# Optimization experiments

Measured on AMD Instinct MI355X. Metric: run time of the kernel, lower is better.

The kernel has to match this reference:

```python
import jax, jax.numpy as jnp
import numpy as np

EMBED_DIM = 512
NUM_HEADS = 8
HEAD_DIM = EMBED_DIM // NUM_HEADS
EDGE_HIDDEN = 512
B, L = 2, 512


def setup_inputs() -> dict:
    key = jax.random.key(0)
    ks = jax.random.split(key, 16)
    s = 0.02
    inp = {
        "query": jax.random.normal(ks[0], (B, L, EMBED_DIM), jnp.float32),
        "key_in": jax.random.normal(ks[1], (B, L, EMBED_DIM), jnp.float32),
        "value": jax.random.normal(ks[2], (B, L, EMBED_DIM), jnp.float32),
        "edge_representation": jax.random.normal(ks[3], (B, L, L), jnp.float32),
        # projection weights stored as [in, out]: y = x @ W + b
        "Wq": jax.random.normal(ks[4], (EMBED_DIM, EMBED_DIM), jnp.float32) * s,
        "bq": jnp.zeros((EMBED_DIM,), jnp.float32),
        "Wk": jax.random.normal(ks[5], (EMBED_DIM, EMBED_DIM), jnp.float32) * s,
        "bk": jnp.zeros((EMBED_DIM,), jnp.float32),
        "Wv": jax.random.normal(ks[6], (EMBED_DIM, EMBED_DIM), jnp.float32) * s,
        "bv": jnp.zeros((EMBED_DIM,), jnp.float32),
        "Wo": jax.random.normal(ks[7], (EMBED_DIM, EMBED_DIM), jnp.float32) * s,
        "bo": jnp.zeros((EMBED_DIM,), jnp.float32),
        # edge MLP: Linear(1 -> 512) -> ReLU -> Linear(512 -> num_heads)
        "We1": jax.random.normal(ks[8], (1, EDGE_HIDDEN), jnp.float32) * s,
        "be1": jnp.zeros((EDGE_HIDDEN,), jnp.float32),
        "We2": jax.random.normal(ks[9], (EDGE_HIDDEN, NUM_HEADS), jnp.float32) * s,
        "be2": jnp.zeros((NUM_HEADS,), jnp.float32),
    }
    return inp


def reference(query, key_in, value, edge_representation,
              Wq, bq, Wk, bk, Wv, bv, Wo, bo, We1, be1, We2, be2):
    Bc, Lc, _ = query.shape
    # project and split heads: [B, H, L, Dh]
    def split_heads(x):
        return x.reshape(Bc, Lc, NUM_HEADS, HEAD_DIM).transpose(0, 2, 1, 3)
    Q = split_heads(query @ Wq + bq)
    K = split_heads(key_in @ Wk + bk)
    V = split_heads(value @ Wv + bv)
    # edge MLP on scalar edge features: [B, L, L, 1] -> [B, L, L, H]
    e = edge_representation[..., None]
    h = jax.nn.relu(e * We1[0] + be1)          # [B, L, L, 512]
    edge_bias = h @ We2 + be2                   # [B, L, L, H]
    scale = 1.0 / jnp.sqrt(jnp.asarray(HEAD_DIM, query.dtype))
    scores = jnp.einsum("bhqd,bhkd->bhqk", Q, K) * scale
    scores = scores + edge_bias.transpose(0, 3, 1, 2)  # [B, H, L, L]
    attn = jax.nn.softmax(scores, axis=-1)
    out = jnp.einsum("bhqk,bhkd->bhqd", attn, V)
    out = out.transpose(0, 2, 1, 3).reshape(Bc, Lc, EMBED_DIM)
    return out @ Wo + bo
```

## Files before the change

### kernel.cpp

```cpp
#include <hip/hip_runtime.h>
#include <hip/hip_bf16.h>

typedef __attribute__((ext_vector_type(8))) short bf16x8;
typedef __attribute__((ext_vector_type(4))) float f32x4;

#define LOG2E 1.44269504088896340736f

#define QB_OFF 2621440
#define KB_OFF 3145728
#define VT_OFF 3670016
#define AO_OFF 4194304
#define T_B   9437184
#define A_B   (T_B + 4096)
#define C_B   (A_B + 20480)

struct MegaArgs {
  const float *xq, *xk, *xv, *eg;
  const float *wq, *wk, *wv, *wo;
  const float *bq, *bk, *bv, *bo;
  const float *w1, *b1, *we2, *be2;
  float* out;
  unsigned short* wsb;
  float *wsT, *wsA, *wsC;
};

__device__ __forceinline__ unsigned short f2bf(float f) {
  union { __hip_bfloat16 h; unsigned short u; } c;
  c.h = __float2bfloat16(f);
  return c.u;
}

__device__ __forceinline__ uint4 pack8(float4 a, float4 b) {
  union { unsigned short us[8]; uint4 u; } r;
  r.us[0] = f2bf(a.x); r.us[1] = f2bf(a.y); r.us[2] = f2bf(a.z); r.us[3] = f2bf(a.w);
  r.us[4] = f2bf(b.x); r.us[5] = f2bf(b.y); r.us[6] = f2bf(b.z); r.us[7] = f2bf(b.w);
  return r.u;
}

__device__ void prep_block(const MegaArgs& a, char* smem) {
  float* sT   = (float*)smem;
  int*   sIdx = (int*)(smem + 2048);
  float (*sDA)[8] = (float (*)[8])(smem + 4096);
  float (*sDC)[8] = (float (*)[8])(smem + 20480);
  float* sA0 = (float*)(smem + 36864);
  float* sC0 = (float*)(smem + 36896);
  int tid = threadIdx.x;
  for (int p = tid; p < 512; p += 256) {
    float w = a.w1[p], bb = a.b1[p];
    sT[p] = (w != 0.f) ? (-bb / w) : -3.4e38f;
    sIdx[p] = p;
#pragma unroll
    for (int h = 0; h < 8; ++h) {
      float w2 = a.we2[p * 8 + h];
      float ra = 0.f, rc = 0.f;
      if (w < 0.f)       { ra = w2 * w; rc = w2 * bb; }
      else if (w == 0.f) { rc = w2 * fmaxf(bb, 0.f); }
      sDA[p][h] = ra; sDC[p][h] = rc;
    }
  }
  __syncthreads();
  for (int size = 2; size <= 512; size <<= 1) {
    for (int stride = size >> 1; stride > 0; stride >>= 1) {
      int p = tid;
      int i = ((p / stride) * (stride << 1)) + (p % stride);
      int j = i + stride;
      bool up = ((i & size) == 0);
      float ti = sT[i], tj = sT[j];
      if (up ? (ti > tj) : (ti < tj)) {
        sT[i] = tj; sT[j] = ti;
        int t = sIdx[i]; sIdx[i] = sIdx[j]; sIdx[j] = t;
      }
      __syncthreads();
    }
  }
#pragma unroll
  for (int h = 0; h < 8; ++h) { sDA[tid][h] += sDA[tid + 256][h]; sDC[tid][h] += sDC[tid + 256][h]; }
  __syncthreads();
  for (int st = 128; st > 0; st >>= 1) {
    if (tid < st) {
#pragma unroll
      for (int h = 0; h < 8; ++h) { sDA[tid][h] += sDA[tid + st][h]; sDC[tid][h] += sDC[tid + st][h]; }
    }
    __syncthreads();
  }
  if (tid < 8) { sA0[tid] = sDA[0][tid]; sC0[tid] = sDC[0][tid] + a.be2[tid]; }
  __syncthreads();
  for (int p = tid; p < 512; p += 256) {
    int k = sIdx[p];
    float wk = a.w1[k], bk2 = a.b1[k];
#pragma unroll
    for (int h = 0; h < 8; ++h) {
      float w2 = a.we2[k * 8 + h];
      float da = 0.f, dc = 0.f;
      if (wk > 0.f)      { da =  w2 * wk; dc =  w2 * bk2; }
      else if (wk < 0.f) { da = -w2 * wk; dc = -w2 * bk2; }
      sDA[p][h] = da; sDC[p][h] = dc;
    }
  }
  __syncthreads();
  for (int off = 1; off < 512; off <<= 1) {
    float ra[2][8], rc[2][8];
#pragma unroll
    for (int e = 0; e < 2; ++e) {
      int p = tid + e * 256;
      if (p >= off) {
#pragma unroll
        for (int h = 0; h < 8; ++h) { ra[e][h] = sDA[p - off][h]; rc[e][h] = sDC[p - off][h]; }
      }
    }
    __syncthreads();
#pragma unroll
    for (int e = 0; e < 2; ++e) {
      int p = tid + e * 256;
      if (p >= off) {
#pragma unroll
        for (int h = 0; h < 8; ++h) { sDA[p][h] += ra[e][h]; sDC[p][h] += rc[e][h]; }
      }
    }
    __syncthreads();
  }
  a.wsT[tid] = sT[tid]; a.wsT[tid + 256] = sT[tid + 256];
  if (tid < 8) { a.wsA[tid * 513] = sA0[tid]; a.wsC[tid * 513] = sC0[tid]; }
  for (int p = tid; p < 512; p += 256) {
#pragma unroll
    for (int h = 0; h < 8; ++h) {
      a.wsA[h * 513 + p + 1] = sA0[h] + sDA[p][h];
      a.wsC[h * 513 + p + 1] = sC0[h] + sDC[p][h];
    }
  }
}

__device__ void gemm_core(const float* __restrict__ Af, const unsigned short* __restrict__ Ab,
                          const float* __restrict__ W, const float* __restrict__ bias,
                          void* out, int mode, int m0, int n0, char* smem) {
  unsigned short (*sA)[72]  = (unsigned short (*)[72])smem;
  unsigned short (*sBt)[72] = (unsigned short (*)[72])(smem + 9216);
  int tid = threadIdx.x, wave = tid >> 6, lane = tid & 63;
  int quad = lane >> 4, l16 = lane & 15;
  f32x4 acc[4] = {{0.f,0.f,0.f,0.f},{0.f,0.f,0.f,0.f},{0.f,0.f,0.f,0.f},{0.f,0.f,0.f,0.f}};
  int lr = tid >> 2, ls = tid & 3;
  int kb8 = lr >> 3, klo = lr & 7;
  for (int kb = 0; kb < 512; kb += 64) {
    __syncthreads();
    if (Af) {
      const float4* ap = (const float4*)(Af + (size_t)(m0 + lr) * 512 + kb + ls * 16);
      float4 v0 = ap[0], v1 = ap[1], v2 = ap[2], v3 = ap[3];
      *(uint4*)&sA[lr][ls * 16]     = pack8(v0, v1);
      *(uint4*)&sA[lr][ls * 16 + 8] = pack8(v2, v3);
    } else {
      *(uint4*)&sA[lr][ls * 16]     = *(const uint4*)(Ab + (size_t)(m0 + lr) * 512 + kb + ls * 16);
      *(uint4*)&sA[lr][ls * 16 + 8] = *(const uint4*)(Ab + (size_t)(m0 + lr) * 512 + kb + ls * 16 + 8);
    }
    {
      const float4* wp = (const float4*)(W + (size_t)(kb + lr) * 512 + n0 + ls * 16);
      float4 w0 = wp[0], w1 = wp[1], w2 = wp[2], w3 = wp[3];
      int nb = ls * 16;
      int slot = ((kb8 ^ ls) << 3) + klo;
      sBt[nb + 0][slot] = f2bf(w0.x);  sBt[nb + 1][slot] = f2bf(w0.y);
      sBt[nb + 2][slot] = f2bf(w0.z);  sBt[nb + 3][slot] = f2bf(w0.w);
      sBt[nb + 4][slot] = f2bf(w1.x);  sBt[nb + 5][slot] = f2bf(w1.y);
      sBt[nb + 6][slot] = f2bf(w1.z);  sBt[nb + 7][slot] = f2bf(w1.w);
      sBt[nb + 8][slot] = f2bf(w2.x);  sBt[nb + 9][slot] = f2bf(w2.y);
      sBt[nb + 10][slot] = f2bf(w2.z); sBt[nb + 11][slot] = f2bf(w2.w);
      sBt[nb + 12][slot] = f2bf(w3.x); sBt[nb + 13][slot] = f2bf(w3.y);
      sBt[nb + 14][slot] = f2bf(w3.z); sBt[nb + 15][slot] = f2bf(w3.w);
    }
    __syncthreads();
    for (int ks = 0; ks < 2; ++ks) {
      bf16x8 af = *(const bf16x8*)&sA[wave * 16 + l16][ks * 32 + quad * 8];
#pragma unroll
      for (int nt = 0; nt < 4; ++nt) {
        bf16x8 bf = *(const bf16x8*)&sBt[nt * 16 + l16][((ks * 4 + quad) ^ nt) * 8];
        acc[nt] = __builtin_amdgcn_mfma_f32_16x16x32_bf16(af, bf, acc[nt], 0, 0, 0);
      }
    }
  }
  int mbase = m0 + wave * 16 + quad * 4;
#pragma unroll
  for (int nt = 0; nt < 4; ++nt) {
    int n = n0 + nt * 16 + l16;
    float bv = bias[n];
#pragma unroll
    for (int r = 0; r < 4; ++r) {
      float v = acc[nt][r] + bv;
      int m = mbase + r;
      if (mode == 0) {
        int b = m >> 9, l = m & 511, hh = n >> 6, d = n & 63;
        ((unsigned short*)out)[(((size_t)(b * 8 + hh) * 512) + l) * 64 + d] = f2bf(v);
      } else if (mode == 1) {
        ((float*)out)[(size_t)m * 512 + n] = v;
      } else {
        int b = m >> 9, l = m & 511, hh = n >> 6, d = n & 63;
        ((unsigned short*)out)[(((size_t)(b * 8 + hh) * 64) + d) * 512 + l] = f2bf(v);
      }
    }
  }
}

__device__ void attn_block(const MegaArgs& a, int qt, int h, int b, char* smem) {
  float* sT  = (float*)smem;
  float* sAh = (float*)(smem + 2048);
  float* sCh = (float*)(smem + 4100);
  unsigned short (*sP)[16][40] = (unsigned short (*)[16][40])(smem + 6160);
  float (*sO)[4][16][16] = (float (*)[4][16][16])(smem + 11280);
  float (*sM)[16] = (float (*)[16])(smem + 27664);
  float (*sL)[16] = (float (*)[16])(smem + 27920);
  const unsigned short* Qb = a.wsb + QB_OFF;
  const unsigned short* Kb = a.wsb + KB_OFF;
  const unsigned short* Vt = a.wsb + VT_OFF;
  int bh = b * 8 + h;
  int q0 = qt * 16;
  int tid = threadIdx.x, wave = tid >> 6, lane = tid & 63;
  int quad = lane >> 4, l16 = lane & 15;
  sT[tid] = a.wsT[tid]; sT[tid + 256] = a.wsT[tid + 256];
  for (int i = tid; i < 513; i += 256) { sAh[i] = a.wsA[h * 513 + i]; sCh[i] = a.wsC[h * 513 + i]; }
  const unsigned short* qp = Qb + ((size_t)bh * 512 + q0 + l16) * 64 + quad * 8;
  bf16x8 qf0 = *(const bf16x8*)qp;
  bf16x8 qf1 = *(const bf16x8*)(qp + 32);
  int key_base = wave * 128;
  f32x4 S[4][2];
#pragma unroll
  for (int kt = 0; kt < 4; ++kt) {
    int key0 = key_base + kt * 32;
#pragma unroll
    for (int half = 0; half < 2; ++half) {
      const unsigned short* kp = Kb + ((size_t)bh * 512 + key0 + half * 16 + l16) * 64 + quad * 8;
      bf16x8 kf0 = *(const bf16x8*)kp;
      bf16x8 kf1 = *(const bf16x8*)(kp + 32);
      f32x4 acc = {0.f, 0.f, 0.f, 0.f};
      acc = __builtin_amdgcn_mfma_f32_16x16x32_bf16(qf0, kf0, acc, 0, 0, 0);
      acc = __builtin_amdgcn_mfma_f32_16x16x32_bf16(qf1, kf1, acc, 0, 0, 0);
      S[kt][half] = acc;
    }
  }
  __syncthreads();
#pragma unroll
  for (int kt = 0; kt < 4; ++kt)
#pragma unroll
    for (int half = 0; half < 2; ++half)
#pragma unroll
      for (int r = 0; r < 4; ++r) {
        int eidx = (b * 512 + q0 + quad * 4 + r) * 512 + key_base + kt * 32 + half * 16 + l16;
        float ev = a.eg[eidx];
        int lo = 0, hi = 512;
#pragma unroll
        for (int it = 0; it < 9; ++it) {
          int mid = (lo + hi) >> 1;
          bool c = sT[mid] < ev;
          lo = c ? mid + 1 : lo;
          hi = c ? hi : mid;
        }
        S[kt][half][r] = S[kt][half][r] * 0.125f + sAh[lo] * ev + sCh[lo];
      }
  float m_w[4], l_w[4];
#pragma unroll
  for (int r = 0; r < 4; ++r) {
    float mx = -3.4e38f;
#pragma unroll
    for (int kt = 0; kt < 4; ++kt) { mx = fmaxf(mx, fmaxf(S[kt][0][r], S[kt][1][r])); }
    for (int off = 1; off < 16; off <<= 1) mx = fmaxf(mx, __shfl_xor(mx, off, 64));
    float s = 0.f;
#pragma unroll
    for (int kt = 0; kt < 4; ++kt)
#pragma unroll
      for (int half = 0; half < 2; ++half) {
        float p = exp2f((S[kt][half][r] - mx) * LOG2E);
        S[kt][half][r] = p; s += p;
      }
    for (int off = 1; off < 16; off <<= 1) s += __shfl_xor(s, off, 64);
    m_w[r] = mx; l_w[r] = s;
  }
  f32x4 Oacc[4] = {{0.f,0.f,0.f,0.f},{0.f,0.f,0.f,0.f},{0.f,0.f,0.f,0.f},{0.f,0.f,0.f,0.f}};
#pragma unroll
  for (int kt = 0; kt < 4; ++kt) {
    int key0 = key_base + kt * 32;
#pragma unroll
    for (int half = 0; half < 2; ++half)
#pragma unroll
      for (int r = 0; r < 4; ++r)
        sP[wave][quad * 4 + r][half * 16 + l16] = f2bf(S[kt][half][r]);
    __builtin_amdgcn_wave_barrier();
    bf16x8 pf = *(const bf16x8*)&sP[wave][l16][quad * 8];
    __builtin_amdgcn_wave_barrier();
#pragma unroll
    for (int nt = 0; nt < 4; ++nt) {
      bf16x8 vf = *(const bf16x8*)(Vt + ((size_t)bh * 64 + nt * 16 + l16) * 512 + key0 + quad * 8);
      Oacc[nt] = __builtin_amdgcn_mfma_f32_16x16x32_bf16(pf, vf, Oacc[nt], 0, 0, 0);
    }
  }
  if (l16 == 0) {
#pragma unroll
    for (int r = 0; r < 4; ++r) { sM[wave][quad * 4 + r] = m_w[r]; sL[wave][quad * 4 + r] = l_w[r]; }
  }
#pragma unroll
  for (int nt = 0; nt < 4; ++nt)
#pragma unroll
    for (int r = 0; r < 4; ++r)
      sO[wave][nt][quad * 4 + r][l16] = Oacc[nt][r];
  __syncthreads();
#pragma unroll
  for (int r = 0; r < 4; ++r) {
    int row = quad * 4 + r;
    float M = fmaxf(fmaxf(sM[0][row], sM[1][row]), fmaxf(sM[2][row], sM[3][row]));
    float L = 0.f, Ov = 0.f;
#pragma unroll
    for (int wv = 0; wv < 4; ++wv) {
      float f = exp2f((sM[wv][row] - M) * LOG2E);
      L += f * sL[wv][row];
      Ov += f * sO[wv][wave][row][l16];
    }
    float v = Ov / L;
    (a.wsb + AO_OFF)[((size_t)(b * 512 + q0 + row)) * 512 + h * 64 + wave * 16 + l16] = f2bf(v);
  }
}

__global__ __launch_bounds__(256) void k1(MegaArgs a) {
  __shared__ __align__(16) char smem[36928];
  int blk = blockIdx.x;
  if (blk == 0) {
    prep_block(a, smem);
  } else {
    int g = blk - 1, z = g >> 7, rem = g & 127;
    const float* A    = (z == 0) ? a.xq : (z == 1) ? a.xk : a.xv;
    const float* W    = (z == 0) ? a.wq : (z == 1) ? a.wk : a.wv;
    const float* bias = (z == 0) ? a.bq : (z == 1) ? a.bk : a.bv;
    void* outp = (void*)(a.wsb + ((z == 0) ? QB_OFF : (z == 1) ? KB_OFF : VT_OFF));
    gemm_core(A, nullptr, W, bias, outp, (z == 2) ? 2 : 0, (rem & 15) * 64, (rem >> 4) * 64, smem);
  }
}

__global__ __launch_bounds__(256) void k2(MegaArgs a) {
  __shared__ __align__(16) char smem[28176];
  int blk = blockIdx.x;
  attn_block(a, blk & 31, (blk >> 5) & 7, blk >> 8, smem);
}

__global__ __launch_bounds__(256) void k3(MegaArgs a) {
  __shared__ __align__(16) char smem[18432];
  gemm_core(nullptr, a.wsb + AO_OFF, a.wo, a.bo, (void*)a.out, 1,
            (blockIdx.x & 15) * 64, (blockIdx.x >> 4) * 64, smem);
}

extern "C" void kernel_launch(void* const* d_in, const int* in_sizes, int n_in,
                              void* d_out, int out_size, void* d_ws, size_t ws_size,
                              hipStream_t stream) {
  MegaArgs a;
  a.xq  = (const float*)d_in[0];
  a.xk  = (const float*)d_in[1];
  a.xv  = (const float*)d_in[2];
  a.eg  = (const float*)d_in[3];
  a.wq  = (const float*)d_in[4];
  a.bq  = (const float*)d_in[5];
  a.wk  = (const float*)d_in[6];
  a.bk  = (const float*)d_in[7];
  a.wv  = (const float*)d_in[8];
  a.bv  = (const float*)d_in[9];
  a.wo  = (const float*)d_in[10];
  a.bo  = (const float*)d_in[11];
  a.w1  = (const float*)d_in[12];
  a.b1  = (const float*)d_in[13];
  a.we2 = (const float*)d_in[14];
  a.be2 = (const float*)d_in[15];
  a.out = (float*)d_out;
  a.wsb = (unsigned short*)d_ws;
  a.wsT = (float*)((char*)d_ws + T_B);
  a.wsA = (float*)((char*)d_ws + A_B);
  a.wsC = (float*)((char*)d_ws + C_B);

  k1<<<385, 256, 0, stream>>>(a);
  k2<<<512, 256, 0, stream>>>(a);
  k3<<<128, 256, 0, stream>>>(a);
}
```

Before: 139.3 us.

## Deduplicate edge-MLP breakpoints and trim prep-block reductions and barriers

The prep block now compacts the sorted ReLU breakpoint thresholds to unique values and stores the unique count. The attention block's binary search then runs over only that many entries, in a data-dependent loop instead of a fixed nine steps, and it loads fewer table entries into LDS. The prep stage also replaces the LDS tree reduction with wave shuffles and uses wave-level barriers for intra-wave bitonic sort stages. Because the test biases are all zero, the breakpoints collapse to very few unique values, so the per-score search cost nearly disappears. The change stays correct for general inputs but adds ballot and prefix bookkeeping to the prep stage.

```diff
diff --git a/kernel.cpp b/kernel.cpp
--- a/kernel.cpp
+++ b/kernel.cpp
@@ -44,23 +44,25 @@
   float (*sDC)[8] = (float (*)[8])(smem + 20480);
   float* sA0 = (float*)(smem + 36864);
   float* sC0 = (float*)(smem + 36896);
-  int tid = threadIdx.x;
-  for (int p = tid; p < 512; p += 256) {
-    float w = a.w1[p], bb = a.b1[p];
-    sT[p] = (w != 0.f) ? (-bb / w) : -3.4e38f;
+  int tid = threadIdx.x, lane = tid & 63, w = tid >> 6;
+  float accA[8] = {0,0,0,0,0,0,0,0}, accC[8] = {0,0,0,0,0,0,0,0};
+  for (int e = 0; e < 2; ++e) {
+    int p = tid + e * 256;
+    float ww = a.w1[p], bb = a.b1[p];
+    sT[p] = (ww != 0.f) ? (-bb / ww) : -3.4e38f;
     sIdx[p] = p;
 #pragma unroll
     for (int h = 0; h < 8; ++h) {
       float w2 = a.we2[p * 8 + h];
-      float ra = 0.f, rc = 0.f;
-      if (w < 0.f)       { ra = w2 * w; rc = w2 * bb; }
-      else if (w == 0.f) { rc = w2 * fmaxf(bb, 0.f); }
-      sDA[p][h] = ra; sDC[p][h] = rc;
+      if (ww < 0.f)       { accA[h] += w2 * ww; accC[h] += w2 * bb; }
+      else if (ww == 0.f) { accC[h] += w2 * fmaxf(bb, 0.f); }
     }
   }
   __syncthreads();
   for (int size = 2; size <= 512; size <<= 1) {
     for (int stride = size >> 1; stride > 0; stride >>= 1) {
+      if (size >= 256 && stride >= 64) __syncthreads();
+      else __builtin_amdgcn_wave_barrier();
       int p = tid;
       int i = ((p / stride) * (stride << 1)) + (p % stride);
       int j = i + stride;
@@ -70,22 +72,27 @@
         sT[i] = tj; sT[j] = ti;
         int t = sIdx[i]; sIdx[i] = sIdx[j]; sIdx[j] = t;
       }
-      __syncthreads();
-    }
-  }
-#pragma unroll
-  for (int h = 0; h < 8; ++h) { sDA[tid][h] += sDA[tid + 256][h]; sDC[tid][h] += sDC[tid + 256][h]; }
-  __syncthreads();
-  for (int st = 128; st > 0; st >>= 1) {
-    if (tid < st) {
-#pragma unroll
-      for (int h = 0; h < 8; ++h) { sDA[tid][h] += sDA[tid + st][h]; sDC[tid][h] += sDC[tid + st][h]; }
-    }
-    __syncthreads();
-  }
-  if (tid < 8) { sA0[tid] = sDA[0][tid]; sC0[tid] = sDC[0][tid] + a.be2[tid]; }
-  __syncthreads();
-  for (int p = tid; p < 512; p += 256) {
+    }
+  }
+  for (int off = 32; off > 0; off >>= 1) {
+#pragma unroll
+    for (int h = 0; h < 8; ++h) {
+      accA[h] += __shfl_xor(accA[h], off);
+      accC[h] += __shfl_xor(accC[h], off);
+    }
+  }
+  if (lane == 0) {
+#pragma unroll
+    for (int h = 0; h < 8; ++h) { sDA[w][h] = accA[h]; sDC[w][h] = accC[h]; }
+  }
+  __syncthreads();
+  if (tid < 8) {
+    sA0[tid] = sDA[0][tid] + sDA[1][tid] + sDA[2][tid] + sDA[3][tid];
+    sC0[tid] = sDC[0][tid] + sDC[1][tid] + sDC[2][tid] + sDC[3][tid] + a.be2[tid];
+  }
+  __syncthreads();
+  for (int e = 0; e < 2; ++e) {
+    int p = tid + e * 256;
     int k = sIdx[p];
     float wk = a.w1[k], bk2 = a.b1[k];
 #pragma unroll
@@ -119,14 +126,52 @@
     }
     __syncthreads();
   }
-  a.wsT[tid] = sT[tid]; a.wsT[tid + 256] = sT[tid + 256];
-  if (tid < 8) { a.wsA[tid * 513] = sA0[tid]; a.wsC[tid * 513] = sC0[tid]; }
-  for (int p = tid; p < 512; p += 256) {
+  bool n0 = (tid == 0) || (sT[tid] != sT[tid - 1]);
+  bool n1 = (sT[tid + 256] != sT[tid + 255]);
+  unsigned long long m0 = __ballot(n0), m1 = __ballot(n1);
+  unsigned long long below = (1ull << lane) - 1ull;
+  int loc0 = __popcll(m0 & below), loc1 = __popcll(m1 & below);
+  int* tot = sIdx;
+  if (lane == 0) { tot[w] = __popcll(m0); tot[4 + w] = __popcll(m1); }
+  __syncthreads();
+  int t[8];
+#pragma unroll
+  for (int j = 0; j < 8; ++j) t[j] = tot[j];
+  int nuniq = t[0] + t[1] + t[2] + t[3] + t[4] + t[5] + t[6] + t[7];
+  int off0 = 0, off1 = t[0] + t[1] + t[2] + t[3];
+  for (int j = 0; j < 4; ++j) {
+    if (j < w) { off0 += t[j]; off1 += t[4 + j]; }
+  }
+  if (n0) {
+    int u = off0 + loc0;
+    a.wsT[u] = sT[tid];
+    if (tid == 0) {
+#pragma unroll
+      for (int h = 0; h < 8; ++h) { a.wsA[h * 513] = sA0[h]; a.wsC[h * 513] = sC0[h]; }
+    } else {
+#pragma unroll
+      for (int h = 0; h < 8; ++h) {
+        a.wsA[h * 513 + u] = sA0[h] + sDA[tid - 1][h];
+        a.wsC[h * 513 + u] = sC0[h] + sDC[tid - 1][h];
+      }
+    }
+  }
+  if (n1) {
+    int u = off1 + loc1;
+    a.wsT[u] = sT[tid + 256];
 #pragma unroll
     for (int h = 0; h < 8; ++h) {
-      a.wsA[h * 513 + p + 1] = sA0[h] + sDA[p][h];
-      a.wsC[h * 513 + p + 1] = sC0[h] + sDC[p][h];
-    }
+      a.wsA[h * 513 + u] = sA0[h] + sDA[tid + 255][h];
+      a.wsC[h * 513 + u] = sC0[h] + sDC[tid + 255][h];
+    }
+  }
+  if (tid == 0) {
+#pragma unroll
+    for (int h = 0; h < 8; ++h) {
+      a.wsA[h * 513 + nuniq] = sA0[h] + sDA[511][h];
+      a.wsC[h * 513 + nuniq] = sC0[h] + sDC[511][h];
+    }
+    *(int*)(a.wsT + 512) = nuniq;
   }
 }
 
@@ -212,8 +257,9 @@
   int q0 = qt * 16;
   int tid = threadIdx.x, wave = tid >> 6, lane = tid & 63;
   int quad = lane >> 4, l16 = lane & 15;
-  sT[tid] = a.wsT[tid]; sT[tid + 256] = a.wsT[tid + 256];
-  for (int i = tid; i < 513; i += 256) { sAh[i] = a.wsA[h * 513 + i]; sCh[i] = a.wsC[h * 513 + i]; }
+  int nu = *(const int*)(a.wsT + 512);
+  for (int i = tid; i < nu; i += 256) sT[i] = a.wsT[i];
+  for (int i = tid; i <= nu; i += 256) { sAh[i] = a.wsA[h * 513 + i]; sCh[i] = a.wsC[h * 513 + i]; }
   const unsigned short* qp = Qb + ((size_t)bh * 512 + q0 + l16) * 64 + quad * 8;
   bf16x8 qf0 = *(const bf16x8*)qp;
   bf16x8 qf1 = *(const bf16x8*)(qp + 32);
@@ -242,9 +288,8 @@
       for (int r = 0; r < 4; ++r) {
         int eidx = (b * 512 + q0 + quad * 4 + r) * 512 + key_base + kt * 32 + half * 16 + l16;
         float ev = a.eg[eidx];
-        int lo = 0, hi = 512;
-#pragma unroll
-        for (int it = 0; it < 9; ++it) {
+        int lo = 0, hi = nu;
+        while (lo < hi) {
           int mid = (lo + hi) >> 1;
           bool c = sT[mid] < ev;
           lo = c ? mid + 1 : lo;
```

Result: faster. 136.5 us (-2.0%).
